# Performance work log

Measured on AMD Instinct MI355X. Metric: run time of the kernel, lower is better.

The kernel has to match this reference:

```python
import jax, jax.numpy as jnp
import numpy as np

B, S, V, CTX, NC, D, NH, L, FF, MAXS = 8, 512, 32000, 8, 512, 256, 4, 4, 512, 512
PAD = 0  # ram_model.pad_token_id


def setup_inputs() -> dict:
    key = jax.random.key(0)
    ks = iter(jax.random.split(key, 64))
    def p(shape, s=0.02):
        return jax.random.normal(next(ks), shape, jnp.float32) * s
    inp = {}
    inp["token_ids"] = jax.random.randint(next(ks), (B, S), 0, V)
    inp["ram_table"] = p((V, NC), 0.1)          # frozen RAM per-cluster scores
    inp["proj_W"] = p((NC, D)); inp["proj_b"] = jnp.zeros((D,), jnp.float32)
    inp["pos_emb"] = p((MAXS, D))
    for pre in ("sa", "ca"):
        for nm in ("Wq", "Wk", "Wv", "Wo"):
            inp[f"{pre}_{nm}"] = p((L, D, D))
        for nm in ("bq", "bk", "bv", "bo"):
            inp[f"{pre}_{nm}"] = jnp.zeros((L, D), jnp.float32)
    for i in (1, 2, 3):
        inp[f"ln{i}_s"] = jnp.ones((L, D), jnp.float32)
        inp[f"ln{i}_b"] = jnp.zeros((L, D), jnp.float32)
    inp["ff_W1"] = p((L, D, FF)); inp["ff_b1"] = jnp.zeros((L, FF), jnp.float32)
    inp["ff_W2"] = p((L, FF, D)); inp["ff_b2"] = jnp.zeros((L, D), jnp.float32)
    inp["out_W"] = p((D, V)); inp["out_b"] = jnp.zeros((V,), jnp.float32)
    return inp


def _ln(x, s, b):
    m = x.mean(-1, keepdims=True)
    v = ((x - m) ** 2).mean(-1, keepdims=True)
    return (x - m) * jax.lax.rsqrt(v + 1e-5) * s + b


def _mha(q_in, k_in, v_in, Wq, bq, Wk, bk, Wv, bv, Wo, bo, mask):
    b, sq, d = q_in.shape
    hd = d // NH
    q = (q_in @ Wq + bq).reshape(b, sq, NH, hd)
    k = (k_in @ Wk + bk).reshape(b, -1, NH, hd)
    v = (v_in @ Wv + bv).reshape(b, -1, NH, hd)
    sc = jnp.einsum("bqhd,bkhd->bhqk", q, k) / np.sqrt(hd).astype(np.float32)
    if mask is not None:
        sc = jnp.where(mask, -1e9, sc)  # mask broadcast over [b, h]
    a = jax.nn.softmax(sc, axis=-1)
    o = jnp.einsum("bhqk,bkhd->bqhd", a, v).reshape(b, sq, d)
    return o @ Wo + bo


def _forward(token_ids, ram_table, proj_W, proj_b, pos_emb,
             sa_Wq, sa_bq, sa_Wk, sa_bk, sa_Wv, sa_bv, sa_Wo, sa_bo,
             ca_Wq, ca_bq, ca_Wk, ca_bk, ca_Wv, ca_bv, ca_Wo, ca_bo,
             ln1_s, ln1_b, ln2_s, ln2_b, ln3_s, ln3_b,
             ff_W1, ff_b1, ff_W2, ff_b2, out_W, out_b):
    b, s = token_ids.shape
    # Batched sliding context windows (replaces the per-position Python loop):
    # left-pad with PAD so window at pos covers [pos-CTX+1, pos].
    padded = jnp.concatenate(
        [jnp.full((b, CTX - 1), PAD, token_ids.dtype), token_ids], axis=1)
    idx = jnp.arange(s)[:, None] + jnp.arange(CTX)[None, :]  # [S, CTX]
    win = padded[:, idx]                                      # [B, S, CTX]
    # Frozen RAM feature extraction: per-cluster scores averaged over window.
    scores = ram_table[win].mean(axis=2)                      # [B, S, NC]
    x = scores @ proj_W + proj_b + pos_emb[:s]                # [B, S, D]
    mask = jnp.triu(jnp.ones((s, s), bool), 1)                # causal
    mem = jnp.zeros((b, 1, D), x.dtype)
    for l in range(L):
        h = _ln(x, ln1_s[l], ln1_b[l])
        x = x + _mha(h, h, h, sa_Wq[l], sa_bq[l], sa_Wk[l], sa_bk[l],
                     sa_Wv[l], sa_bv[l], sa_Wo[l], sa_bo[l], mask)
        h = _ln(x, ln2_s[l], ln2_b[l])
        x = x + _mha(h, mem, mem, ca_Wq[l], ca_bq[l], ca_Wk[l], ca_bk[l],
                     ca_Wv[l], ca_bv[l], ca_Wo[l], ca_bo[l], None)
        h = _ln(x, ln3_s[l], ln3_b[l])
        x = x + jax.nn.relu(h @ ff_W1[l] + ff_b1[l]) @ ff_W2[l] + ff_b2[l]
    return x @ out_W + out_b                                  # [B, S, V]


def reference(token_ids, ram_table, proj_W, proj_b, pos_emb,
              sa_Wq, sa_bq, sa_Wk, sa_bk, sa_Wv, sa_bv, sa_Wo, sa_bo,
              ca_Wq, ca_bq, ca_Wk, ca_bk, ca_Wv, ca_bv, ca_Wo, ca_bo,
              ln1_s, ln1_b, ln2_s, ln2_b, ln3_s, ln3_b,
              ff_W1, ff_b1, ff_W2, ff_b2, out_W, out_b):
    return _forward(token_ids, ram_table, proj_W, proj_b, pos_emb,
                    sa_Wq, sa_bq, sa_Wk, sa_bk, sa_Wv, sa_bv, sa_Wo, sa_bo,
                    ca_Wq, ca_bq, ca_Wk, ca_bk, ca_Wv, ca_bv, ca_Wo, ca_bo,
                    ln1_s, ln1_b, ln2_s, ln2_b, ln3_s, ln3_b,
                    ff_W1, ff_b1, ff_W2, ff_b2, out_W, out_b)
```

## Files before the change

### kernel.cpp

```cpp
#include <hip/hip_runtime.h>

#define B_   8
#define S_   512
#define V_   32000
#define CTX_ 8
#define NC_  512
#define D_   256
#define NH_  4
#define L_   4
#define FF_  512
#define HD_  64
#define BS_  4096

#define FG_F32   1
#define FG_BF16  2
#define FG_RELU  4
#define FG_POS   8
#define FG_NT    16
#define FG_QKV   32

typedef __attribute__((ext_vector_type(8))) short bf16x8;
typedef __attribute__((ext_vector_type(4))) float f32x4;

__device__ inline void gload16(const void* g, void* lds) {
    __builtin_amdgcn_global_load_lds(
        (const __attribute__((address_space(1))) void*)g,
        (__attribute__((address_space(3))) void*)lds, 16, 0, 0);
}

__device__ inline ushort f2b(float f) {
    union { float f; unsigned u; } v; v.f = f;
    unsigned u = v.u;
    unsigned r = u + 0x7fffu + ((u >> 16) & 1u);
    return (ushort)(r >> 16);
}

__global__ __launch_bounds__(256) void prologue_kernel(
    const int* __restrict__ tok, const float* __restrict__ ram,
    const float* __restrict__ proj_W, const float* __restrict__ Wq,
    const float* __restrict__ Wk, const float* __restrict__ Wv,
    const float* __restrict__ Wo, const float* __restrict__ W1,
    const float* __restrict__ W2, const float* __restrict__ outW,
    const float* __restrict__ ca_bv, const float* __restrict__ ca_Wo,
    const float* __restrict__ ca_bo, const float* __restrict__ bq,
    const float* __restrict__ bk, const float* __restrict__ bv,
    ushort* __restrict__ pjWb, ushort* __restrict__ WqkvB,
    ushort* __restrict__ WoB, ushort* __restrict__ ff1B,
    ushort* __restrict__ ff2B, ushort* __restrict__ Wb,
    float* __restrict__ cc, float* __restrict__ qkvb,
    ushort* __restrict__ scores)
{
    __shared__ float tile[32 * 33];
    int id = blockIdx.x;
    int t = threadIdx.x;
    if (id < 10176) {
        const float* src; ushort* dst; int K, N, lt;
        if (id < 128)       { src = proj_W; dst = pjWb; K = 512; N = 256; lt = id; }
        else if (id < 896)  { lt = id - 128; int z = lt >> 6; lt &= 63;
                              int which = z / L_, l = z % L_;
                              src = (which == 0 ? Wq : which == 1 ? Wk : Wv) + (size_t)l * 65536;
                              dst = WqkvB + ((size_t)l * 768 + which * 256) * 256;
                              K = 256; N = 256; }
        else if (id < 1152) { lt = id - 896; int l = lt >> 6; lt &= 63;
                              src = Wo + (size_t)l * 65536; dst = WoB + (size_t)l * 65536;
                              K = 256; N = 256; }
        else if (id < 1664) { lt = id - 1152; int l = lt >> 7; lt &= 127;
                              src = W1 + (size_t)l * 131072; dst = ff1B + (size_t)l * 131072;
                              K = 256; N = 512; }
        else if (id < 2176) { lt = id - 1664; int l = lt >> 7; lt &= 127;
                              src = W2 + (size_t)l * 131072; dst = ff2B + (size_t)l * 131072;
                              K = 512; N = 256; }
        else                { lt = id - 2176; src = outW; dst = Wb; K = 256; N = 32000; }
        int ntc = N >> 5;
        int n0 = (lt % ntc) * 32, k0 = (lt / ntc) * 32;
        int tx = t & 31, ty = t >> 5;
        for (int i = ty; i < 32; i += 8)
            tile[i * 33 + tx] = src[(size_t)(k0 + i) * N + n0 + tx];
        __syncthreads();
        for (int i = ty; i < 32; i += 8)
            dst[(size_t)(n0 + i) * K + k0 + tx] = f2b(tile[tx * 33 + i]);
    } else if (id < 10180) {
        int l = id - 10176;
        const float* w = ca_Wo + (size_t)l * D_ * D_;
        const float* b = ca_bv + l * D_;
        float acc = 0.f;
        for (int d = 0; d < D_; ++d) acc += b[d] * w[(size_t)d * D_ + t];
        cc[l * D_ + t] = acc + ca_bo[l * D_ + t];
        for (int u = t; u < 768; u += 256) {
            int which = u >> 8, c = u & 255;
            const float* src = which == 0 ? bq : which == 1 ? bk : bv;
            qkvb[l * 768 + u] = src[l * 256 + c];
        }
    } else {
        int bs = id - 10180;
        int b = bs >> 9, s = bs & 511;
        float a0 = 0.f, a1 = 0.f;
        #pragma unroll
        for (int c = 0; c < CTX_; ++c) {
            int pos = s + c - (CTX_ - 1);
            int tk = (pos < 0) ? 0 : tok[b * S_ + pos];
            const float* row = ram + (size_t)tk * NC_;
            a0 += row[t];
            a1 += row[t + 256];
        }
        scores[(size_t)bs * NC_ + t]       = f2b(a0 * 0.125f);
        scores[(size_t)bs * NC_ + t + 256] = f2b(a1 * 0.125f);
    }
}

__global__ __launch_bounds__(256) void ln_bf16_kernel(
    const float* __restrict__ x, const float* __restrict__ sc,
    const float* __restrict__ bi, ushort* __restrict__ out)
{
    int row = blockIdx.x * 4 + (threadIdx.x >> 6);
    int lane = threadIdx.x & 63;
    float4 v = *reinterpret_cast<const float4*>(x + (size_t)row * D_ + lane * 4);
    float s = v.x + v.y + v.z + v.w;
    float s2 = v.x * v.x + v.y * v.y + v.z * v.z + v.w * v.w;
    #pragma unroll
    for (int o = 32; o > 0; o >>= 1) {
        s  += __shfl_xor(s, o);
        s2 += __shfl_xor(s2, o);
    }
    float mean = s * (1.f / D_);
    float var = s2 * (1.f / D_) - mean * mean;
    float r = rsqrtf(var + 1e-5f);
    float4 g = *reinterpret_cast<const float4*>(sc + lane * 4);
    float4 bb = *reinterpret_cast<const float4*>(bi + lane * 4);
    ushort4 o4;
    o4.x = f2b((v.x - mean) * r * g.x + bb.x);
    o4.y = f2b((v.y - mean) * r * g.y + bb.y);
    o4.z = f2b((v.z - mean) * r * g.z + bb.z);
    o4.w = f2b((v.w - mean) * r * g.w + bb.w);
    *reinterpret_cast<ushort4*>(out + (size_t)row * D_ + lane * 4) = o4;
}

template<int BM, int BN, int K, int TN, int FLAGS>
__global__ __launch_bounds__(256) void gemm_t(
    const ushort* __restrict__ A, const ushort* __restrict__ Bt,
    const float* __restrict__ bias, const float* __restrict__ extra,
    const float* __restrict__ resid, const float* __restrict__ pos,
    float* __restrict__ Cf, ushort* __restrict__ Cb)
{
    constexpr int WM = BM / 32;
    constexpr int WN = BN / 32;
    constexpr int MT = 4096 / BM;
    constexpr int NWG = MT * (TN / BN);
    __shared__ ushort smem[(BM + BN) * 64];
    ushort* As = smem;
    ushort* Bs = smem + BM * 64;
    int bid = blockIdx.x;
    int swz = bid;
    if constexpr ((NWG & 7) == 0) {
        constexpr int cpx = NWG >> 3;
        swz = (bid & 7) * cpx + (bid >> 3);
    }
    int mt = swz % MT, nt = swz / MT;
    int row0 = mt * BM, col0 = nt * BN;
    int t = threadIdx.x, w = t >> 6, lane = t & 63;
    int wr = w >> 1, wc = w & 1;
    int srow = lane >> 3, slot = lane & 7;
    int gcol = (slot ^ srow) * 8;

    f32x4 acc[WM][WN] = {};
    int sl = lane >> 4;
    int rA0 = wr * (BM / 2) + (lane & 15);
    int rB0 = wc * (BN / 2) + (lane & 15);

    #pragma unroll
    for (int k0 = 0; k0 < K; k0 += 64) {
        #pragma unroll
        for (int c = 0; c < BM / 32; ++c) {
            int chunk = w * (BM / 32) + c;
            gload16(A + (size_t)(row0 + chunk * 8 + srow) * K + k0 + gcol,
                    As + chunk * 512);
        }
        #pragma unroll
        for (int c = 0; c < BN / 32; ++c) {
            int chunk = w * (BN / 32) + c;
            gload16(Bt + (size_t)(col0 + chunk * 8 + srow) * K + k0 + gcol,
                    Bs + chunk * 512);
        }
        __syncthreads();
        #pragma unroll
        for (int kk = 0; kk < 2; ++kk) {
            bf16x8 a[WM], b[WN];
            #pragma unroll
            for (int m = 0; m < WM; ++m) {
                int rr = rA0 + m * 16;
                a[m] = *reinterpret_cast<const bf16x8*>(
                    As + rr * 64 + (((sl + kk * 4) ^ (rr & 7)) * 8));
            }
            #pragma unroll
            for (int n = 0; n < WN; ++n) {
                int rr = rB0 + n * 16;
                b[n] = *reinterpret_cast<const bf16x8*>(
                    Bs + rr * 64 + (((sl + kk * 4) ^ (rr & 7)) * 8));
            }
            #pragma unroll
            for (int m = 0; m < WM; ++m)
                #pragma unroll
                for (int n = 0; n < WN; ++n)
                    acc[m][n] = __builtin_amdgcn_mfma_f32_16x16x32_bf16(
                        a[m], b[n], acc[m][n], 0, 0, 0);
        }
        __syncthreads();
    }

    int lr = (lane >> 4) * 4;
    int lc = lane & 15;

    if constexpr (FLAGS & FG_NT) {
        float* Ct = reinterpret_cast<float*>(smem);
        #pragma unroll
        for (int p = 0; p < 2; ++p) {
            __syncthreads();
            if (wr == p) {
                #pragma unroll
                for (int n = 0; n < WN; ++n) {
                    int colL = wc * (BN / 2) + n * 16 + lc;
                    float bn = bias[col0 + colL];
                    #pragma unroll
                    for (int m = 0; m < WM; ++m)
                        #pragma unroll
                        for (int r = 0; r < 4; ++r)
                            Ct[(m * 16 + lr + r) * BN + colL] = acc[m][n][r] + bn;
                }
            }
            __syncthreads();
            constexpr int NV4 = (BM / 2) * (BN / 4);
            #pragma unroll
            for (int j = 0; j < NV4 / 256; ++j) {
                int idx = t + j * 256;
                int rl = idx / (BN / 4);
                int c4 = idx % (BN / 4);
                f32x4 v4 = reinterpret_cast<const f32x4*>(Ct)[idx];
                __builtin_nontemporal_store(v4,
                    reinterpret_cast<f32x4*>(
                        &Cf[(size_t)(row0 + p * (BM / 2) + rl) * TN + col0 + c4 * 4]));
            }
        }
        return;
    }

    #pragma unroll
    for (int n = 0; n < WN; ++n) {
        int col = col0 + wc * (BN / 2) + n * 16 + lc;
        float bn = bias ? bias[col] : 0.f;
        float en = extra ? extra[col] : 0.f;
        #pragma unroll
        for (int m = 0; m < WM; ++m) {
            int rbase = row0 + wr * (BM / 2) + m * 16 + lr;
            #pragma unroll
            for (int r = 0; r < 4; ++r) {
                int row = rbase + r;
                float v = acc[m][n][r] + bn;
                if constexpr (FLAGS & FG_QKV) {
                    int which = col >> 8;
                    int c2 = col & 255;
                    int hh = c2 >> 6, dd = c2 & 63;
                    int bb = row >> 9, ss = row & 511;
                    if (which == 0) {
                        Cb[((((size_t)bb * NH_ + hh) * S_ + ss) << 6) + dd] =
                            f2b(v * 0.125f);
                    } else if (which == 1) {
                        (Cb + 1048576)[((((size_t)bb * NH_ + hh) * S_ + ss) << 6) + dd] =
                            f2b(v);
                    } else {
                        (Cb + 2097152)[((((size_t)bb * NH_ + hh) * HD_ + dd) << 9) + ss] =
                            f2b(v);
                    }
                } else {
                    if constexpr (FLAGS & FG_POS) v += pos[(size_t)(row & 511) * TN + col];
                    if (extra) v += en;
                    if (resid) v += resid[(size_t)row * TN + col];
                    if constexpr (FLAGS & FG_RELU) v = fmaxf(v, 0.f);
                    if constexpr (FLAGS & FG_BF16)
                        Cb[(size_t)row * TN + col] = f2b(v);
                    if constexpr (FLAGS & FG_F32)
                        Cf[(size_t)row * TN + col] = v;
                }
            }
        }
    }
}

__global__ __launch_bounds__(256) void attn_kernel(
    const ushort* __restrict__ q, const ushort* __restrict__ k,
    const ushort* __restrict__ vT, ushort* __restrict__ pv)
{
    int qt = blockIdx.x, bh = blockIdx.y;
    __shared__ ushort smem[20480];
    ushort* Ps = smem + 16384;
    int t = threadIdx.x, w = t >> 6, lane = t & 63;
    int srow = lane >> 3, slot = lane & 7;
    int gcol = (slot ^ srow) * 8;
    int sl = lane >> 4, lc = lane & 15;

    const ushort* Qp = q + ((size_t)bh * S_ + qt * 64) * HD_;
    const ushort* Kp = k + (size_t)bh * S_ * HD_;
    const ushort* Vp = vT + (size_t)bh * HD_ * S_;

    int qrow = w * 16 + lc;
    bf16x8 qf0 = *reinterpret_cast<const bf16x8*>(Qp + qrow * 64 + sl * 8);
    bf16x8 qf1 = *reinterpret_cast<const bf16x8*>(Qp + qrow * 64 + sl * 8 + 32);

    f32x4 o[4] = {};
    float m_r[4], l_r[4];
    #pragma unroll
    for (int r = 0; r < 4; ++r) { m_r[r] = -1e30f; l_r[r] = 0.f; }
    int row_abs = qt * 64 + w * 16 + sl * 4;

    {
        ushort* Ks = smem;
        ushort* Vs = smem + 4096;
        #pragma unroll
        for (int c = 0; c < 2; ++c) {
            int chunk = w * 2 + c;
            gload16(Kp + (size_t)(chunk * 8 + srow) * 64 + gcol, Ks + chunk * 512);
            gload16(Vp + (size_t)(chunk * 8 + srow) * 512 + gcol, Vs + chunk * 512);
        }
    }

    for (int kt = 0; kt <= qt; ++kt) {
        int cur = kt & 1;
        ushort* Ks = smem + cur * 8192;
        ushort* Vs = smem + cur * 8192 + 4096;
        __syncthreads();
        if (kt < qt) {
            ushort* Kn = smem + (cur ^ 1) * 8192;
            ushort* Vn = Kn + 4096;
            #pragma unroll
            for (int c = 0; c < 2; ++c) {
                int chunk = w * 2 + c;
                gload16(Kp + (size_t)((kt + 1) * 64 + chunk * 8 + srow) * 64 + gcol,
                        Kn + chunk * 512);
                gload16(Vp + (size_t)(chunk * 8 + srow) * 512 + (kt + 1) * 64 + gcol,
                        Vn + chunk * 512);
            }
        }

        f32x4 sa[4] = {};
        #pragma unroll
        for (int n = 0; n < 4; ++n) {
            int rB = n * 16 + lc;
            bf16x8 b0 = *reinterpret_cast<const bf16x8*>(
                Ks + rB * 64 + ((sl ^ (rB & 7)) * 8));
            bf16x8 b1 = *reinterpret_cast<const bf16x8*>(
                Ks + rB * 64 + (((sl + 4) ^ (rB & 7)) * 8));
            sa[n] = __builtin_amdgcn_mfma_f32_16x16x32_bf16(qf0, b0, sa[n], 0, 0, 0);
            sa[n] = __builtin_amdgcn_mfma_f32_16x16x32_bf16(qf1, b1, sa[n], 0, 0, 0);
        }
        if (kt == qt) {
            #pragma unroll
            for (int n = 0; n < 4; ++n) {
                int col = kt * 64 + n * 16 + lc;
                #pragma unroll
                for (int r = 0; r < 4; ++r)
                    if (col > row_abs + r) sa[n][r] = -1e30f;
            }
        }
        float psum[4];
        #pragma unroll
        for (int r = 0; r < 4; ++r) {
            float vm = fmaxf(fmaxf(sa[0][r], sa[1][r]), fmaxf(sa[2][r], sa[3][r]));
            vm = fmaxf(vm, __shfl_xor(vm, 1));
            vm = fmaxf(vm, __shfl_xor(vm, 2));
            vm = fmaxf(vm, __shfl_xor(vm, 4));
            vm = fmaxf(vm, __shfl_xor(vm, 8));
            float mn = fmaxf(m_r[r], vm);
            float scl = __expf(m_r[r] - mn);
            m_r[r] = mn;
            l_r[r] *= scl;
            #pragma unroll
            for (int n = 0; n < 4; ++n) o[n][r] *= scl;
            psum[r] = 0.f;
        }
        ushort* Pw = Ps + w * 1024;
        #pragma unroll
        for (int n = 0; n < 4; ++n) {
            #pragma unroll
            for (int r = 0; r < 4; ++r) {
                float p = __expf(sa[n][r] - m_r[r]);
                psum[r] += p;
                int prow = sl * 4 + r;
                int pcol = n * 16 + lc;
                int pslot = pcol >> 3;
                Pw[prow * 64 + ((pslot ^ (prow & 7)) * 8) + (pcol & 7)] = f2b(p);
            }
        }
        #pragma unroll
        for (int r = 0; r < 4; ++r) {
            float s = psum[r];
            s += __shfl_xor(s, 1);
            s += __shfl_xor(s, 2);
            s += __shfl_xor(s, 4);
            s += __shfl_xor(s, 8);
            l_r[r] += s;
        }
        int arow = lc;
        bf16x8 pa0 = *reinterpret_cast<const bf16x8*>(
            Pw + arow * 64 + ((sl ^ (arow & 7)) * 8));
        bf16x8 pa1 = *reinterpret_cast<const bf16x8*>(
            Pw + arow * 64 + (((sl + 4) ^ (arow & 7)) * 8));
        #pragma unroll
        for (int n = 0; n < 4; ++n) {
            int rB = n * 16 + lc;
            bf16x8 v0 = *reinterpret_cast<const bf16x8*>(
                Vs + rB * 64 + ((sl ^ (rB & 7)) * 8));
            bf16x8 v1 = *reinterpret_cast<const bf16x8*>(
                Vs + rB * 64 + (((sl + 4) ^ (rB & 7)) * 8));
            o[n] = __builtin_amdgcn_mfma_f32_16x16x32_bf16(pa0, v0, o[n], 0, 0, 0);
            o[n] = __builtin_amdgcn_mfma_f32_16x16x32_bf16(pa1, v1, o[n], 0, 0, 0);
        }
    }

    int bb = bh >> 2, hh = bh & 3;
    #pragma unroll
    for (int r = 0; r < 4; ++r) {
        float inv = 1.f / l_r[r];
        int ss = qt * 64 + w * 16 + sl * 4 + r;
        #pragma unroll
        for (int n = 0; n < 4; ++n) {
            int dd = n * 16 + lc;
            pv[((size_t)bb * S_ + ss) * D_ + hh * HD_ + dd] = f2b(o[n][r] * inv);
        }
    }
}

extern "C" void kernel_launch(void* const* d_in, const int* in_sizes, int n_in,
                              void* d_out, int out_size, void* d_ws, size_t ws_size,
                              hipStream_t stream)
{
    const int*   tok     = (const int*)  d_in[0];
    const float* ram     = (const float*)d_in[1];
    const float* proj_W  = (const float*)d_in[2];
    const float* proj_b  = (const float*)d_in[3];
    const float* pos_emb = (const float*)d_in[4];
    const float* sa_Wq   = (const float*)d_in[5];
    const float* sa_Wk   = (const float*)d_in[6];
    const float* sa_Wv   = (const float*)d_in[7];
    const float* sa_Wo   = (const float*)d_in[8];
    const float* sa_bq   = (const float*)d_in[9];
    const float* sa_bk   = (const float*)d_in[10];
    const float* sa_bv   = (const float*)d_in[11];
    const float* sa_bo   = (const float*)d_in[12];
    const float* ca_Wo   = (const float*)d_in[16];
    const float* ca_bv   = (const float*)d_in[19];
    const float* ca_bo   = (const float*)d_in[20];
    const float* ln1_s   = (const float*)d_in[21];
    const float* ln1_b   = (const float*)d_in[22];
    const float* ln3_s   = (const float*)d_in[25];
    const float* ln3_b   = (const float*)d_in[26];
    const float* ff_W1   = (const float*)d_in[27];
    const float* ff_b1   = (const float*)d_in[28];
    const float* ff_W2   = (const float*)d_in[29];
    const float* ff_b2   = (const float*)d_in[30];
    const float* out_W   = (const float*)d_in[31];
    const float* out_b   = (const float*)d_in[32];

    float* out = (float*)d_out;
    float* ws  = (float*)d_ws;

    float*  x   = ws;
    float*  cc  = ws + (size_t)BS_ * D_;
    ushort* xb  = (ushort*)(cc + L_ * D_);
    ushort* Wb  = xb + (size_t)BS_ * D_;

    ushort* sc_b  = (ushort*)out;
    ushort* h_b   = sc_b + 2097152;
    ushort* qkv3  = h_b + 1048576;
    ushort* pv_b  = qkv3 + 3145728;
    ushort* ffh_b = pv_b + 1048576;
    ushort* pjWb  = ffh_b + 2097152;
    ushort* WqkvB = pjWb + 131072;
    ushort* WoB   = WqkvB + 786432;
    ushort* ff1B  = WoB + 262144;
    ushort* ff2B  = ff1B + 524288;
    float*  qkvb  = (float*)(ff2B + 524288);
    ushort* qb_b  = qkv3;
    ushort* kb_b  = qkv3 + 1048576;
    ushort* vT_b  = qkv3 + 2097152;

    prologue_kernel<<<14276, 256, 0, stream>>>(
        tok, ram, proj_W, sa_Wq, sa_Wk, sa_Wv, sa_Wo, ff_W1, ff_W2, out_W,
        ca_bv, ca_Wo, ca_bo, sa_bq, sa_bk, sa_bv,
        pjWb, WqkvB, WoB, ff1B, ff2B, Wb, cc, qkvb, sc_b);

    gemm_t<64, 64, 512, 256, FG_F32 | FG_POS><<<256, 256, 0, stream>>>(
        sc_b, pjWb, proj_b, nullptr, nullptr, pos_emb, x, nullptr);

    for (int l = 0; l < L_; ++l) {
        ln_bf16_kernel<<<1024, 256, 0, stream>>>(x, ln1_s + l * D_, ln1_b + l * D_, h_b);
        gemm_t<64, 64, 256, 768, FG_QKV><<<768, 256, 0, stream>>>(
            h_b, WqkvB + (size_t)l * 196608, qkvb + l * 768,
            nullptr, nullptr, nullptr, nullptr, qkv3);
        attn_kernel<<<dim3(8, 32), 256, 0, stream>>>(qb_b, kb_b, vT_b, pv_b);
        gemm_t<64, 64, 256, 256, FG_F32><<<256, 256, 0, stream>>>(
            pv_b, WoB + (size_t)l * 65536, sa_bo + l * D_,
            cc + l * D_, x, nullptr, x, nullptr);
        ln_bf16_kernel<<<1024, 256, 0, stream>>>(x, ln3_s + l * D_, ln3_b + l * D_, h_b);
        gemm_t<64, 64, 256, 512, FG_BF16 | FG_RELU><<<512, 256, 0, stream>>>(
            h_b, ff1B + (size_t)l * 131072, ff_b1 + l * FF_,
            nullptr, nullptr, nullptr, nullptr, ffh_b);
        if (l < L_ - 1) {
            gemm_t<64, 64, 512, 256, FG_F32><<<256, 256, 0, stream>>>(
                ffh_b, ff2B + (size_t)l * 131072, ff_b2 + l * D_,
                nullptr, x, nullptr, x, nullptr);
        } else {
            gemm_t<64, 64, 512, 256, FG_BF16><<<256, 256, 0, stream>>>(
                ffh_b, ff2B + (size_t)l * 131072, ff_b2 + l * D_,
                nullptr, x, nullptr, nullptr, xb);
        }
    }

    gemm_t<128, 128, 256, 32000, FG_F32 | FG_NT><<<8000, 256, 0, stream>>>(
        xb, Wb, out_b, nullptr, nullptr, nullptr, out, nullptr);
}
```

Baseline: 400.0 us.

## Fuse LayerNorm into full-row N=256 GEMM epilogues

Adds a gemm_row kernel in which each block computes 16 full output rows (all 256 columns) with MFMA. It applies bias, residual and positional terms, then performs the row LayerNorm in the epilogue, writing both the fp32 residual stream and the bf16 normalized activations. This replaces the standalone LayerNorm launches and the extra read of x they required. The trade is a smaller M tile, so the full weight matrix is reloaded by every block and there is less data reuse per block. Xout aliasing resid is safe because each element is read and then written by the same thread.

```diff
diff --git a/kernel.cpp b/kernel.cpp
--- a/kernel.cpp
+++ b/kernel.cpp
@@ -108,31 +108,106 @@
     }
 }
 
-__global__ __launch_bounds__(256) void ln_bf16_kernel(
-    const float* __restrict__ x, const float* __restrict__ sc,
-    const float* __restrict__ bi, ushort* __restrict__ out)
+template<int K, int FLAGS>
+__global__ __launch_bounds__(256) void gemm_row(
+    const ushort* __restrict__ A, const ushort* __restrict__ Bt,
+    const float* __restrict__ bias, const float* __restrict__ extra,
+    const float* __restrict__ resid, const float* __restrict__ pos,
+    const float* __restrict__ lnS, const float* __restrict__ lnB,
+    float* __restrict__ Xout, ushort* __restrict__ Hout)
 {
-    int row = blockIdx.x * 4 + (threadIdx.x >> 6);
-    int lane = threadIdx.x & 63;
-    float4 v = *reinterpret_cast<const float4*>(x + (size_t)row * D_ + lane * 4);
-    float s = v.x + v.y + v.z + v.w;
-    float s2 = v.x * v.x + v.y * v.y + v.z * v.z + v.w * v.w;
-    #pragma unroll
-    for (int o = 32; o > 0; o >>= 1) {
-        s  += __shfl_xor(s, o);
-        s2 += __shfl_xor(s2, o);
-    }
-    float mean = s * (1.f / D_);
-    float var = s2 * (1.f / D_) - mean * mean;
-    float r = rsqrtf(var + 1e-5f);
-    float4 g = *reinterpret_cast<const float4*>(sc + lane * 4);
-    float4 bb = *reinterpret_cast<const float4*>(bi + lane * 4);
-    ushort4 o4;
-    o4.x = f2b((v.x - mean) * r * g.x + bb.x);
-    o4.y = f2b((v.y - mean) * r * g.y + bb.y);
-    o4.z = f2b((v.z - mean) * r * g.z + bb.z);
-    o4.w = f2b((v.w - mean) * r * g.w + bb.w);
-    *reinterpret_cast<ushort4*>(out + (size_t)row * D_ + lane * 4) = o4;
+    __shared__ ushort As[16 * 64];
+    __shared__ ushort Bs[256 * 64];
+    __shared__ float red[2][4][16];
+    int mt = blockIdx.x;
+    int row0 = mt * 16;
+    int t = threadIdx.x, w = t >> 6, lane = t & 63;
+    int srow = lane >> 3, slot = lane & 7;
+    int gcol = (slot ^ srow) * 8;
+    int sl = lane >> 4, lc = lane & 15;
+    int rA = lane & 15;
+
+    f32x4 acc[4] = {};
+
+    #pragma unroll
+    for (int k0 = 0; k0 < K; k0 += 64) {
+        if (w < 2)
+            gload16(A + (size_t)(row0 + w * 8 + srow) * K + k0 + gcol, As + w * 512);
+        #pragma unroll
+        for (int c = 0; c < 8; ++c) {
+            int chunk = w * 8 + c;
+            gload16(Bt + (size_t)(chunk * 8 + srow) * K + k0 + gcol, Bs + chunk * 512);
+        }
+        __syncthreads();
+        #pragma unroll
+        for (int kk = 0; kk < 2; ++kk) {
+            bf16x8 a = *reinterpret_cast<const bf16x8*>(
+                As + rA * 64 + (((sl + kk * 4) ^ (rA & 7)) * 8));
+            #pragma unroll
+            for (int n = 0; n < 4; ++n) {
+                int rr = w * 64 + n * 16 + lc;
+                rr = w * 64 + (lane & 15) + n * 16;
+                bf16x8 b = *reinterpret_cast<const bf16x8*>(
+                    Bs + rr * 64 + (((sl + kk * 4) ^ (rr & 7)) * 8));
+                acc[n] = __builtin_amdgcn_mfma_f32_16x16x32_bf16(a, b, acc[n], 0, 0, 0);
+            }
+        }
+        __syncthreads();
+    }
+
+    float v[4][4];
+    float psum[4] = {}, psq[4] = {};
+    #pragma unroll
+    for (int n = 0; n < 4; ++n) {
+        int col = w * 64 + n * 16 + lc;
+        float bn = bias[col];
+        float en = extra ? extra[col] : 0.f;
+        #pragma unroll
+        for (int r = 0; r < 4; ++r) {
+            int row = row0 + sl * 4 + r;
+            float x = acc[n][r] + bn;
+            if constexpr (FLAGS & FG_POS) x += pos[(size_t)(row & 511) * D_ + col];
+            x += en;
+            if (resid) x += resid[(size_t)row * D_ + col];
+            v[n][r] = x;
+            psum[r] += x;
+            psq[r] += x * x;
+        }
+    }
+    #pragma unroll
+    for (int r = 0; r < 4; ++r) {
+        #pragma unroll
+        for (int o = 8; o > 0; o >>= 1) {
+            psum[r] += __shfl_xor(psum[r], o);
+            psq[r]  += __shfl_xor(psq[r], o);
+        }
+    }
+    if (lc == 0) {
+        #pragma unroll
+        for (int r = 0; r < 4; ++r) {
+            red[0][w][sl * 4 + r] = psum[r];
+            red[1][w][sl * 4 + r] = psq[r];
+        }
+    }
+    __syncthreads();
+    #pragma unroll
+    for (int r = 0; r < 4; ++r) {
+        int rl = sl * 4 + r;
+        float s  = red[0][0][rl] + red[0][1][rl] + red[0][2][rl] + red[0][3][rl];
+        float s2 = red[1][0][rl] + red[1][1][rl] + red[1][2][rl] + red[1][3][rl];
+        float mean = s * (1.f / D_);
+        float var = s2 * (1.f / D_) - mean * mean;
+        float rstd = rsqrtf(var + 1e-5f);
+        int row = row0 + rl;
+        #pragma unroll
+        for (int n = 0; n < 4; ++n) {
+            int col = w * 64 + n * 16 + lc;
+            float x = v[n][r];
+            Xout[(size_t)row * D_ + col] = x;
+            Hout[(size_t)row * D_ + col] =
+                f2b((x - mean) * rstd * lnS[col] + lnB[col]);
+        }
+    }
 }
 
 template<int BM, int BN, int K, int TN, int FLAGS>
@@ -487,26 +562,26 @@
         ca_bv, ca_Wo, ca_bo, sa_bq, sa_bk, sa_bv,
         pjWb, WqkvB, WoB, ff1B, ff2B, Wb, cc, qkvb, sc_b);
 
-    gemm_t<64, 64, 512, 256, FG_F32 | FG_POS><<<256, 256, 0, stream>>>(
-        sc_b, pjWb, proj_b, nullptr, nullptr, pos_emb, x, nullptr);
+    gemm_row<512, FG_POS><<<256, 256, 0, stream>>>(
+        sc_b, pjWb, proj_b, nullptr, nullptr, pos_emb,
+        ln1_s, ln1_b, x, h_b);
 
     for (int l = 0; l < L_; ++l) {
-        ln_bf16_kernel<<<1024, 256, 0, stream>>>(x, ln1_s + l * D_, ln1_b + l * D_, h_b);
         gemm_t<64, 64, 256, 768, FG_QKV><<<768, 256, 0, stream>>>(
             h_b, WqkvB + (size_t)l * 196608, qkvb + l * 768,
             nullptr, nullptr, nullptr, nullptr, qkv3);
         attn_kernel<<<dim3(8, 32), 256, 0, stream>>>(qb_b, kb_b, vT_b, pv_b);
-        gemm_t<64, 64, 256, 256, FG_F32><<<256, 256, 0, stream>>>(
+        gemm_row<256, 0><<<256, 256, 0, stream>>>(
             pv_b, WoB + (size_t)l * 65536, sa_bo + l * D_,
-            cc + l * D_, x, nullptr, x, nullptr);
-        ln_bf16_kernel<<<1024, 256, 0, stream>>>(x, ln3_s + l * D_, ln3_b + l * D_, h_b);
+            cc + l * D_, x, nullptr, ln3_s + l * D_, ln3_b + l * D_, x, h_b);
         gemm_t<64, 64, 256, 512, FG_BF16 | FG_RELU><<<512, 256, 0, stream>>>(
             h_b, ff1B + (size_t)l * 131072, ff_b1 + l * FF_,
             nullptr, nullptr, nullptr, nullptr, ffh_b);
         if (l < L_ - 1) {
-            gemm_t<64, 64, 512, 256, FG_F32><<<256, 256, 0, stream>>>(
+            gemm_row<512, 0><<<256, 256, 0, stream>>>(
                 ffh_b, ff2B + (size_t)l * 131072, ff_b2 + l * D_,
-                nullptr, x, nullptr, x, nullptr);
+                nullptr, x, nullptr, ln1_s + (l + 1) * D_, ln1_b + (l + 1) * D_,
+                x, h_b);
         } else {
             gemm_t<64, 64, 512, 256, FG_BF16><<<256, 256, 0, stream>>>(
                 ffh_b, ff2B + (size_t)l * 131072, ff_b2 + l * D_,
```

Result: faster. 389.2 us (-2.7%).
